# Kernel optimization log

Measured on AMD Instinct MI355X. Metric: run time of the kernel, lower is better.

## Reference

```python
import jax, jax.numpy as jnp
import numpy as np

EMBED_DIM = 1024
NUM_HEADS = 16
HEAD_DIM = EMBED_DIM // NUM_HEADS
TGT_LEN, BSZ = 2048, 4


def setup_inputs() -> dict:
    key = jax.random.key(0)
    ks = jax.random.split(key, 12)
    s = 1.0 / np.sqrt(EMBED_DIM)
    inp = {
        "query": jax.random.normal(ks[0], (TGT_LEN, BSZ, EMBED_DIM), jnp.float32),
        "key": jax.random.normal(ks[1], (TGT_LEN, BSZ, EMBED_DIM), jnp.float32),
        "value": jax.random.normal(ks[2], (TGT_LEN, BSZ, EMBED_DIM), jnp.float32),
        # nn.Linear weights: [out, in], y = x @ W.T + b
        "Wq": jax.random.normal(ks[3], (EMBED_DIM, EMBED_DIM), jnp.float32) * s,
        "bq": jax.random.normal(ks[4], (EMBED_DIM,), jnp.float32) * s,
        "Wk": jax.random.normal(ks[5], (EMBED_DIM, EMBED_DIM), jnp.float32) * s,
        "bk": jax.random.normal(ks[6], (EMBED_DIM,), jnp.float32) * s,
        "Wv": jax.random.normal(ks[7], (EMBED_DIM, EMBED_DIM), jnp.float32) * s,
        "bv": jax.random.normal(ks[8], (EMBED_DIM,), jnp.float32) * s,
        "Wo": jax.random.normal(ks[9], (EMBED_DIM, EMBED_DIM), jnp.float32) * s,
        "bo": jax.random.normal(ks[10], (EMBED_DIM,), jnp.float32) * s,
    }
    return inp


def _split_heads(x, seq_len, bsz):
    # [S, B, E] -> [B*H, S, Dh]
    return x.reshape(seq_len, bsz * NUM_HEADS, HEAD_DIM).transpose(1, 0, 2)


def reference(query, key, value, Wq, bq, Wk, bk, Wv, bv, Wo, bo):
    tgt_len, bsz, embed_dim = query.shape
    src_len = key.shape[0]
    q = query @ Wq.T + bq
    k = key @ Wk.T + bk
    v = value @ Wv.T + bv
    q = _split_heads(q, tgt_len, bsz)   # [B*H, T, Dh]
    k = _split_heads(k, src_len, bsz)   # [B*H, S, Dh]
    v = _split_heads(v, src_len, bsz)   # [B*H, S, Dh]
    scale = 1.0 / np.sqrt(HEAD_DIM).astype(np.float32)
    attn_weights = jnp.einsum('btd,bsd->bts', q, k) * scale  # [B*H, T, S]
    attn_weights = jax.nn.softmax(attn_weights, axis=-1)
    attn = jnp.einsum('bts,bsd->btd', attn_weights, v)       # [B*H, T, Dh]
    attn = attn.transpose(1, 0, 2).reshape(tgt_len, bsz, embed_dim)
    return attn @ Wo.T + bo
```

## Files before the change

kernel.cpp:

```cpp
#include <hip/hip_runtime.h>
#include <stdint.h>

#define TGT 2048
#define BSZQ 4
#define EMB 1024
#define NHEAD 16
#define DH 64
#define BH 64
#define MROWS 8192

using short8 = __attribute__((ext_vector_type(8))) short;
using f32x4  = __attribute__((ext_vector_type(4))) float;
using u32x2  = __attribute__((ext_vector_type(2))) unsigned int;
typedef unsigned short u16;
typedef unsigned int u32;

#define QSCALE 0.18033688011112042f

__device__ __forceinline__ u16 f2bf(float f) {
  union { float f; u32 u; } v; v.f = f;
  return (u16)((v.u + 0x7fffu + ((v.u >> 16) & 1u)) >> 16);
}
__device__ __forceinline__ u32 packbf(float a, float b) {
  union { float f; u32 u; } x, y; x.f = a; y.f = b;
  return __builtin_amdgcn_perm(y.u + 0x8000u, x.u + 0x8000u, 0x07060302u);
}
__device__ __forceinline__ f32x4 mfma16(short8 a, short8 b, f32x4 c) {
  return __builtin_amdgcn_mfma_f32_16x16x32_bf16(a, b, c, 0, 0, 0);
}
__device__ __forceinline__ void gload_lds16(const u16* g, u16* l) {
  __builtin_amdgcn_global_load_lds((const __attribute__((address_space(1))) void*)g,
                                   (__attribute__((address_space(3))) void*)l,
                                   16, 0, 0);
}

__global__ __launch_bounds__(256)
void cvt3(const float* __restrict__ a, const float* __restrict__ b, const float* __restrict__ c,
          u16* __restrict__ oa, u16* __restrict__ ob, u16* __restrict__ oc)
{
  const float* s; u16* d;
  if (blockIdx.y == 0) { s = a; d = oa; }
  else if (blockIdx.y == 1) { s = b; d = ob; }
  else { s = c; d = oc; }
  const int i = (blockIdx.x * 256 + threadIdx.x) * 8;
  float4 v0 = *(const float4*)(s + i);
  float4 v1 = *(const float4*)(s + i + 4);
  union { u16 h[8]; short8 v; } r;
  r.h[0] = f2bf(v0.x); r.h[1] = f2bf(v0.y); r.h[2] = f2bf(v0.z); r.h[3] = f2bf(v0.w);
  r.h[4] = f2bf(v1.x); r.h[5] = f2bf(v1.y); r.h[6] = f2bf(v1.z); r.h[7] = f2bf(v1.w);
  *(short8*)(d + i) = r.v;
}
__global__ __launch_bounds__(256)
void cvt4(const float* __restrict__ a, const float* __restrict__ b,
          const float* __restrict__ c, const float* __restrict__ e,
          u16* __restrict__ oa, u16* __restrict__ ob, u16* __restrict__ oc, u16* __restrict__ oe)
{
  const float* s; u16* d;
  if (blockIdx.y == 0) { s = a; d = oa; }
  else if (blockIdx.y == 1) { s = b; d = ob; }
  else if (blockIdx.y == 2) { s = c; d = oc; }
  else { s = e; d = oe; }
  const int i = (blockIdx.x * 256 + threadIdx.x) * 8;
  float4 v0 = *(const float4*)(s + i);
  float4 v1 = *(const float4*)(s + i + 4);
  union { u16 h[8]; short8 v; } r;
  r.h[0] = f2bf(v0.x); r.h[1] = f2bf(v0.y); r.h[2] = f2bf(v0.z); r.h[3] = f2bf(v0.w);
  r.h[4] = f2bf(v1.x); r.h[5] = f2bf(v1.y); r.h[6] = f2bf(v1.z); r.h[7] = f2bf(v1.w);
  *(short8*)(d + i) = r.v;
}

__device__ __forceinline__
void gemm_body(const u16* __restrict__ A, const u16* __restrict__ W,
               const float* __restrict__ bias, void* __restrict__ outp,
               u16* As, u16* Bs, int mode)
{
  const int tid = threadIdx.x;
  const int wave = tid >> 6, lane = tid & 63;
  const int col16 = lane & 15, quad = lane >> 4;
  const int m0 = blockIdx.y * 128, n0 = blockIdx.x * 128;
  const int wr = (wave >> 1) * 64;
  const int wc = (wave & 1) * 64;
  const int sr = lane >> 3;
  const int sg = (lane & 7) ^ sr;
  const int fk = col16 & 7;

#define GSTAGE(K0, CB) do { \
  _Pragma("unroll") for (int s_ = 0; s_ < 4; ++s_) \
    gload_lds16(A + (size_t)(m0 + wave * 32 + s_ * 8 + sr) * EMB + (K0) + sg * 8, \
                &As[(CB) * 8192 + (wave * 32 + s_ * 8) * 64]); \
  _Pragma("unroll") for (int s_ = 0; s_ < 4; ++s_) \
    gload_lds16(W + (size_t)(n0 + wave * 32 + s_ * 8 + sr) * EMB + (K0) + sg * 8, \
                &Bs[(CB) * 8192 + (wave * 32 + s_ * 8) * 64]); \
} while (0)

  f32x4 acc[4][4];
#pragma unroll
  for (int i = 0; i < 4; ++i)
#pragma unroll
    for (int j = 0; j < 4; ++j) acc[i][j] = (f32x4)0.0f;

  GSTAGE(0, 0);
  for (int kt = 0; kt < EMB / 64; ++kt) {
    const int cb = kt & 1;
    __syncthreads();
    if (kt < EMB / 64 - 1) GSTAGE((kt + 1) * 64, cb ^ 1);
    short8 af[4][2], bfr[4][2];
#pragma unroll
    for (int kk = 0; kk < 2; ++kk) {
#pragma unroll
      for (int i = 0; i < 4; ++i)
        af[i][kk] = *(const short8*)&As[cb * 8192 + (wr + i * 16 + col16) * 64
                                        + (((kk * 4 + quad) ^ fk) << 3)];
#pragma unroll
      for (int j = 0; j < 4; ++j)
        bfr[j][kk] = *(const short8*)&Bs[cb * 8192 + (wc + j * 16 + col16) * 64
                                         + (((kk * 4 + quad) ^ fk) << 3)];
    }
#pragma unroll
    for (int i = 0; i < 4; ++i)
#pragma unroll
      for (int j = 0; j < 4; ++j) {
        acc[i][j] = mfma16(af[i][0], bfr[j][0], acc[i][j]);
        acc[i][j] = mfma16(af[i][1], bfr[j][1], acc[i][j]);
      }
  }
#undef GSTAGE

  const int rowb = quad * 4;
#pragma unroll
  for (int i = 0; i < 4; ++i) {
#pragma unroll
    for (int j = 0; j < 4; ++j) {
      const int gn = n0 + wc + j * 16 + col16;
      const float bia = bias[gn];
      const int h = gn >> 6, d = gn & 63;
#pragma unroll
      for (int r = 0; r < 4; ++r) {
        const int gm = m0 + wr + i * 16 + rowb + r;
        float val = acc[i][j][r] + bia;
        const int t = gm >> 2, b = gm & 3;
        if (mode == 0) {
          ((u16*)outp)[((size_t)(b * NHEAD + h) * TGT + t) * DH + d] = f2bf(val * QSCALE);
        } else if (mode == 1) {
          ((u16*)outp)[((size_t)(b * NHEAD + h) * TGT + t) * DH + d] = f2bf(val);
        } else if (mode == 2) {
          const int p = (t & ~63) + ((t & 15) << 2) + ((t >> 4) & 3);
          ((u16*)outp)[((size_t)(b * NHEAD + h) * DH + d) * TGT + p] = f2bf(val);
        } else {
          ((float*)outp)[(size_t)gm * EMB + gn] = val;
        }
      }
    }
  }
}

__global__ __launch_bounds__(256, 2)
void gemm_qkv(const u16* __restrict__ qb, const u16* __restrict__ kb, const u16* __restrict__ vb,
              const u16* __restrict__ wq, const u16* __restrict__ wk, const u16* __restrict__ wv,
              const float* __restrict__ bq, const float* __restrict__ bk, const float* __restrict__ bv,
              u16* __restrict__ qh, u16* __restrict__ kh, u16* __restrict__ vtp)
{
  __shared__ u16 As[2 * 8192];
  __shared__ u16 Bs[2 * 8192];
  const int z = blockIdx.z;
  const u16* A = (z == 0) ? qb : (z == 1) ? kb : vb;
  const u16* W = (z == 0) ? wq : (z == 1) ? wk : wv;
  const float* bias = (z == 0) ? bq : (z == 1) ? bk : bv;
  void* outp = (z == 0) ? (void*)qh : (z == 1) ? (void*)kh : (void*)vtp;
  gemm_body(A, W, bias, outp, As, Bs, z);
}

__global__ __launch_bounds__(256, 2)
void gemm_o(const u16* __restrict__ A, const u16* __restrict__ W,
            const float* __restrict__ bias, float* __restrict__ outp)
{
  __shared__ u16 As[2 * 8192];
  __shared__ u16 Bs[2 * 8192];
  gemm_body(A, W, bias, (void*)outp, As, Bs, 3);
}

__global__ __launch_bounds__(256, 2)
void flash_attn(const u16* __restrict__ qh, const u16* __restrict__ kh,
                const u16* __restrict__ vtp, u16* __restrict__ ao)
{
  __shared__ u16 Ks[2 * 128 * 64];
  __shared__ u16 Vs[2 * 64 * 128];
  __shared__ u16 Ps[128 * 64];

  const int tid = threadIdx.x;
  const int wave = tid >> 6, lane = tid & 63;
  const int col16 = lane & 15, quad = lane >> 4;
  const int id = blockIdx.x;
  const int bh = (id & 7) * 8 + (id >> 7);
  const int q0 = ((id >> 3) & 15) * 128;
  const int wq0 = q0 + wave * 32;

  const u16* qbase = qh + (size_t)bh * TGT * DH;
  const u16* kbase = kh + (size_t)bh * TGT * DH;
  const u16* vbase = vtp + (size_t)bh * DH * TGT;

  const int krl = lane >> 3;
  const int kgl = (lane & 7) ^ krl;
  const int vdl = wave * 4 + quad;
  const int vgl = (lane & 15) ^ vdl;

#define STAGE(S0, B) do { \
  _Pragma("unroll") for (int t_ = 0; t_ < 4; ++t_) { \
    gload_lds16(kbase + (size_t)((S0) + t_ * 32 + wave * 8 + krl) * DH + kgl * 8, \
                &Ks[(B) * 8192 + (t_ * 32 + wave * 8) * 64]); \
    gload_lds16(vbase + (size_t)(t_ * 16 + vdl) * TGT + (S0) + vgl * 8, \
                &Vs[(B) * 8192 + (t_ * 16 + wave * 4) * 128]); \
  } } while (0)

  short8 qf[2][2];
#pragma unroll
  for (int i = 0; i < 2; ++i)
#pragma unroll
    for (int kk = 0; kk < 2; ++kk)
      qf[i][kk] = *(const short8*)(qbase + (size_t)(wq0 + i * 16 + col16) * DH + kk * 32 + quad * 8);

  f32x4 oacc[2][4];
  float lsum[2][4];
#pragma unroll
  for (int i = 0; i < 2; ++i)
#pragma unroll
    for (int j = 0; j < 4; ++j) oacc[i][j] = (f32x4)0.0f;
#pragma unroll
  for (int i = 0; i < 2; ++i)
#pragma unroll
    for (int r = 0; r < 4; ++r) lsum[i][r] = 0.0f;

  STAGE(0, 0);

  for (int st = 0; st < TGT / 128; ++st) {
    const int cb = st & 1;
    __syncthreads();
    if (st < TGT / 128 - 1) STAGE((st + 1) * 128, cb ^ 1);

#pragma unroll
    for (int half = 0; half < 2; ++half) {
      u32 pka[2][4][2];
#pragma unroll
      for (int jpL = 0; jpL < 2; ++jpL) {
        f32x4 s[2][2];
#pragma unroll
        for (int jh = 0; jh < 2; ++jh) {
          const int j = half * 4 + jpL * 2 + jh;
          const int R = j * 16 + col16;
          short8 kf0 = *(const short8*)&Ks[cb * 8192 + R * 64 + ((quad ^ (col16 & 7)) << 3)];
          short8 kf1 = *(const short8*)&Ks[cb * 8192 + R * 64 + (((quad + 4) ^ (col16 & 7)) << 3)];
#pragma unroll
          for (int i = 0; i < 2; ++i) {
            f32x4 t0 = mfma16(qf[i][0], kf0, (f32x4)0.0f);
            s[i][jh] = mfma16(qf[i][1], kf1, t0);
          }
        }
#pragma unroll
        for (int i = 0; i < 2; ++i)
#pragma unroll
          for (int r = 0; r < 4; ++r) {
            float p0 = __builtin_amdgcn_exp2f(s[i][0][r]);
            float p1 = __builtin_amdgcn_exp2f(s[i][1][r]);
            lsum[i][r] += p0 + p1;
            pka[i][r][jpL] = packbf(p0, p1);
          }
      }
#pragma unroll
      for (int i = 0; i < 2; ++i)
#pragma unroll
        for (int r = 0; r < 4; ++r) {
          const int row = wave * 32 + i * 16 + quad * 4 + r;
          u32x2 w2; w2[0] = pka[i][r][0]; w2[1] = pka[i][r][1];
          *(u32x2*)&Ps[row * 64 + (((col16 >> 1) ^ (row & 7)) << 3) + ((col16 & 1) << 2)] = w2;
        }
#pragma unroll
      for (int ks = 0; ks < 2; ++ks) {
        short8 pf[2];
#pragma unroll
        for (int i = 0; i < 2; ++i) {
          const int row = wave * 32 + i * 16 + col16;
          pf[i] = *(const short8*)&Ps[row * 64 + (((ks * 4 + quad) ^ (col16 & 7)) << 3)];
        }
#pragma unroll
        for (int jd = 0; jd < 4; ++jd) {
          const int d = jd * 16 + col16;
          short8 vf = *(const short8*)&Vs[cb * 8192 + d * 128
                                          + (((half * 8 + ks * 4 + quad) ^ col16) << 3)];
#pragma unroll
          for (int i = 0; i < 2; ++i)
            oacc[i][jd] = mfma16(pf[i], vf, oacc[i][jd]);
        }
      }
    }
  }
#undef STAGE

#pragma unroll
  for (int i = 0; i < 2; ++i)
#pragma unroll
    for (int r = 0; r < 4; ++r) {
#pragma unroll
      for (int off = 1; off < 16; off <<= 1)
        lsum[i][r] += __shfl_xor(lsum[i][r], off, 64);
      lsum[i][r] = __builtin_amdgcn_rcpf(lsum[i][r]);
    }
  const int b = bh >> 4, h = bh & 15;
#pragma unroll
  for (int i = 0; i < 2; ++i)
#pragma unroll
    for (int jd = 0; jd < 4; ++jd)
#pragma unroll
      for (int r = 0; r < 4; ++r) {
        const int t = q0 + wave * 32 + i * 16 + quad * 4 + r;
        const int d = jd * 16 + col16;
        ao[((size_t)t * BSZQ + b) * EMB + h * DH + d] = f2bf(oacc[i][jd][r] * lsum[i][r]);
      }
}

extern "C" void kernel_launch(void* const* d_in, const int* in_sizes, int n_in,
                              void* d_out, int out_size, void* d_ws, size_t ws_size,
                              hipStream_t stream) {
  const float* query = (const float*)d_in[0];
  const float* key   = (const float*)d_in[1];
  const float* value = (const float*)d_in[2];
  const float* Wq = (const float*)d_in[3];
  const float* bq = (const float*)d_in[4];
  const float* Wk = (const float*)d_in[5];
  const float* bk = (const float*)d_in[6];
  const float* Wv = (const float*)d_in[7];
  const float* bv = (const float*)d_in[8];
  const float* Wo = (const float*)d_in[9];
  const float* bo = (const float*)d_in[10];

  const size_t BIG = (size_t)MROWS * EMB;
  const size_t WSZ = (size_t)EMB * EMB;
  u16* buf0 = (u16*)d_ws;
  u16* buf1 = buf0 + BIG;
  u16* buf2 = buf1 + BIG;
  u16* buf3 = buf2 + BIG;
  u16* wqb  = buf3 + BIG;
  u16* wkb  = wqb + WSZ;
  u16* wvb  = wkb + WSZ;
  u16* wob  = wvb + WSZ;

  cvt3<<<dim3(BIG / 2048, 3), 256, 0, stream>>>(query, key, value, buf0, buf1, buf2);
  cvt4<<<dim3(WSZ / 2048, 4), 256, 0, stream>>>(Wq, Wk, Wv, Wo, wqb, wkb, wvb, wob);

  gemm_qkv<<<dim3(EMB / 128, MROWS / 128, 3), 256, 0, stream>>>(
      buf0, buf1, buf2, wqb, wkb, wvb, bq, bk, bv,
      buf3 , buf0 , buf1 );

  flash_attn<<<1024, 256, 0, stream>>>(buf3, buf0, buf1, buf2);

  gemm_o<<<dim3(EMB / 128, MROWS / 128), 256, 0, stream>>>(buf2, wob, bo, (float*)d_out);
}
```

Baseline: 401.2 us.

## Single-buffer GEMM LDS for higher occupancy, swizzle block order, fix aliasing

The QKV and output GEMMs drop LDS double buffering, which halves shared memory per block, and raise launch bounds from 2 to 4 blocks per CU. Blocks are also remapped so consecutive block IDs spread across M tiles and share weight columns, aiming for better L2 reuse. K and V head outputs now go to the output buffer instead of overwriting the QKV inputs, which removes a read-after-write race between blocks. The cost is that global-to-LDS loads are no longer overlapped with MFMA within a block, and latency hiding now depends on the extra occupancy.

Result: faster. 374.0 us (-6.8%).

```diff
diff --git a/kernel.cpp b/kernel.cpp
--- a/kernel.cpp
+++ b/kernel.cpp
@@ -72,25 +72,24 @@
 __device__ __forceinline__
 void gemm_body(const u16* __restrict__ A, const u16* __restrict__ W,
                const float* __restrict__ bias, void* __restrict__ outp,
-               u16* As, u16* Bs, int mode)
+               u16* As, u16* Bs, int mode, int m0, int n0)
 {
   const int tid = threadIdx.x;
   const int wave = tid >> 6, lane = tid & 63;
   const int col16 = lane & 15, quad = lane >> 4;
-  const int m0 = blockIdx.y * 128, n0 = blockIdx.x * 128;
   const int wr = (wave >> 1) * 64;
   const int wc = (wave & 1) * 64;
   const int sr = lane >> 3;
   const int sg = (lane & 7) ^ sr;
   const int fk = col16 & 7;
 
-#define GSTAGE(K0, CB) do { \
+#define GSTAGE(K0) do { \
   _Pragma("unroll") for (int s_ = 0; s_ < 4; ++s_) \
     gload_lds16(A + (size_t)(m0 + wave * 32 + s_ * 8 + sr) * EMB + (K0) + sg * 8, \
-                &As[(CB) * 8192 + (wave * 32 + s_ * 8) * 64]); \
+                &As[(wave * 32 + s_ * 8) * 64]); \
   _Pragma("unroll") for (int s_ = 0; s_ < 4; ++s_) \
     gload_lds16(W + (size_t)(n0 + wave * 32 + s_ * 8 + sr) * EMB + (K0) + sg * 8, \
-                &Bs[(CB) * 8192 + (wave * 32 + s_ * 8) * 64]); \
+                &Bs[(wave * 32 + s_ * 8) * 64]); \
 } while (0)
 
   f32x4 acc[4][4];
@@ -99,21 +98,20 @@
 #pragma unroll
     for (int j = 0; j < 4; ++j) acc[i][j] = (f32x4)0.0f;
 
-  GSTAGE(0, 0);
   for (int kt = 0; kt < EMB / 64; ++kt) {
-    const int cb = kt & 1;
+    if (kt) __syncthreads();
+    GSTAGE(kt * 64);
     __syncthreads();
-    if (kt < EMB / 64 - 1) GSTAGE((kt + 1) * 64, cb ^ 1);
     short8 af[4][2], bfr[4][2];
 #pragma unroll
     for (int kk = 0; kk < 2; ++kk) {
 #pragma unroll
       for (int i = 0; i < 4; ++i)
-        af[i][kk] = *(const short8*)&As[cb * 8192 + (wr + i * 16 + col16) * 64
+        af[i][kk] = *(const short8*)&As[(wr + i * 16 + col16) * 64
                                         + (((kk * 4 + quad) ^ fk) << 3)];
 #pragma unroll
       for (int j = 0; j < 4; ++j)
-        bfr[j][kk] = *(const short8*)&Bs[cb * 8192 + (wc + j * 16 + col16) * 64
+        bfr[j][kk] = *(const short8*)&Bs[(wc + j * 16 + col16) * 64
                                          + (((kk * 4 + quad) ^ fk) << 3)];
     }
 #pragma unroll
@@ -154,29 +152,38 @@
   }
 }
 
-__global__ __launch_bounds__(256, 2)
+__global__ __launch_bounds__(256, 4)
 void gemm_qkv(const u16* __restrict__ qb, const u16* __restrict__ kb, const u16* __restrict__ vb,
               const u16* __restrict__ wq, const u16* __restrict__ wk, const u16* __restrict__ wv,
               const float* __restrict__ bq, const float* __restrict__ bk, const float* __restrict__ bv,
               u16* __restrict__ qh, u16* __restrict__ kh, u16* __restrict__ vtp)
 {
-  __shared__ u16 As[2 * 8192];
-  __shared__ u16 Bs[2 * 8192];
-  const int z = blockIdx.z;
+  __shared__ u16 As[8192];
+  __shared__ u16 Bs[8192];
+  const int lin = ((int)blockIdx.z * 64 + blockIdx.y) * 8 + blockIdx.x;
+  const int swz = (lin & 7) * 192 + (lin >> 3);
+  const int n0 = (swz & 7) * 128;
+  const int tmp = swz >> 3;
+  const int m0 = (tmp & 63) * 128;
+  const int z = tmp >> 6;
   const u16* A = (z == 0) ? qb : (z == 1) ? kb : vb;
   const u16* W = (z == 0) ? wq : (z == 1) ? wk : wv;
   const float* bias = (z == 0) ? bq : (z == 1) ? bk : bv;
   void* outp = (z == 0) ? (void*)qh : (z == 1) ? (void*)kh : (void*)vtp;
-  gemm_body(A, W, bias, outp, As, Bs, z);
-}
-
-__global__ __launch_bounds__(256, 2)
+  gemm_body(A, W, bias, outp, As, Bs, z, m0, n0);
+}
+
+__global__ __launch_bounds__(256, 4)
 void gemm_o(const u16* __restrict__ A, const u16* __restrict__ W,
             const float* __restrict__ bias, float* __restrict__ outp)
 {
-  __shared__ u16 As[2 * 8192];
-  __shared__ u16 Bs[2 * 8192];
-  gemm_body(A, W, bias, (void*)outp, As, Bs, 3);
+  __shared__ u16 As[8192];
+  __shared__ u16 Bs[8192];
+  const int lin = (int)blockIdx.y * 8 + blockIdx.x;
+  const int swz = (lin & 7) * 64 + (lin >> 3);
+  const int n0 = (swz & 7) * 128;
+  const int m0 = (swz >> 3) * 128;
+  gemm_body(A, W, bias, (void*)outp, As, Bs, 3, m0, n0);
 }
 
 __global__ __launch_bounds__(256, 2)
@@ -342,15 +349,17 @@
   u16* wkb  = wqb + WSZ;
   u16* wvb  = wkb + WSZ;
   u16* wob  = wvb + WSZ;
+  u16* khs  = (u16*)d_out;
+  u16* vts  = khs + BIG;
 
   cvt3<<<dim3(BIG / 2048, 3), 256, 0, stream>>>(query, key, value, buf0, buf1, buf2);
   cvt4<<<dim3(WSZ / 2048, 4), 256, 0, stream>>>(Wq, Wk, Wv, Wo, wqb, wkb, wvb, wob);
 
   gemm_qkv<<<dim3(EMB / 128, MROWS / 128, 3), 256, 0, stream>>>(
       buf0, buf1, buf2, wqb, wkb, wvb, bq, bk, bv,
-      buf3 , buf0 , buf1 );
-
-  flash_attn<<<1024, 256, 0, stream>>>(buf3, buf0, buf1, buf2);
+      buf3 , khs , vts );
+
+  flash_attn<<<1024, 256, 0, stream>>>(buf3, khs, vts, buf2);
 
   gemm_o<<<dim3(EMB / 128, MROWS / 128), 256, 0, stream>>>(buf2, wob, bo, (float*)d_out);
 }
```
